# Kernel optimization log

Hardware: AMD Instinct MI355X
Metric: run time of the kernel (lower is better)

Reference implementation:

```python
import jax, jax.numpy as jnp
import numpy as np

N_LAYERS = 4
B, L, D = 2, 2048, 512
H, E = 8, 64          # n_heads = d_model // d_head
DFF = 1024
EPS = 1e-6
MAX_LOG_SCALE = float(np.log(100.0))   # QKNorm max_scale clamp
LOG10 = float(np.log(10.0))            # QKNorm scale init


def rms_norm(x, scale, eps=EPS):
    # matches torch rms_norm: x * (scale * rsqrt(mean(x^2, -1) + eps))
    ms = jnp.mean(jnp.square(x), axis=-1, keepdims=True)
    return x * (scale * jax.lax.rsqrt(ms + eps))


def rope(x):
    # standard rotary embedding over head dim, half-split convention. x: [n,h,l,e]
    e, l = x.shape[-1], x.shape[-2]
    inv = 1.0 / (10000.0 ** (jnp.arange(0, e, 2, dtype=jnp.float32) / e))
    freqs = jnp.arange(l, dtype=jnp.float32)[:, None] * inv[None, :]   # [l, e/2]
    cos, sin = jnp.cos(freqs), jnp.sin(freqs)
    x1, x2 = x[..., : e // 2], x[..., e // 2:]
    return jnp.concatenate([x1 * cos - x2 * sin, x1 * sin + x2 * cos], axis=-1)


def setup_inputs() -> dict:
    key = jax.random.key(0)
    ks = jax.random.split(key, 10)
    s = 0.02
    return {
        "x": jax.random.normal(ks[0], (B, L, D), jnp.float32),
        "cond": jax.random.normal(ks[1], (B, D), jnp.float32),
        "attn_mask": jnp.ones((B, L), jnp.int32),
        # per-layer stacked params (torch Linear(in,out,bias=False) stored as [in,out], y = x @ W)
        "wn_attn": s * jax.random.normal(ks[2], (N_LAYERS, D, D), jnp.float32),      # AdaRMSNorm cond proj (attn)
        "wqkv": s * jax.random.normal(ks[3], (N_LAYERS, D, 3 * D), jnp.float32),
        "qk_scale": jnp.full((N_LAYERS, H), LOG10, jnp.float32),                     # QKNorm per-head log-scale
        "wout": s * jax.random.normal(ks[4], (N_LAYERS, D, D), jnp.float32),
        "wn_ff": s * jax.random.normal(ks[5], (N_LAYERS, D, D), jnp.float32),        # AdaRMSNorm cond proj (ff)
        "wup": s * jax.random.normal(ks[6], (N_LAYERS, D, 2 * DFF), jnp.float32),
        "wdown": s * jax.random.normal(ks[7], (N_LAYERS, DFF, D), jnp.float32),
        "out_scale": jnp.ones((D,), jnp.float32),                                    # final RMSNorm scale
    }


def forward(x, cond, attn_mask, wn_attn, wqkv, qk_scale, wout, wn_ff, wup, wdown, out_scale):
    n, l, d = x.shape
    # mask bias: (attn_mask != 1) * -1e9, repeated 'n l -> n h l s' (query-dim mask, as in source)
    bias = (attn_mask != 1).astype(x.dtype) * -1e9
    bias = bias[:, None, :, None]  # [n,1,l,1] broadcast over heads and key dim

    def block(h_x, p):
        wn_a, w_qkv, qs, w_o, wn_f, w_up, w_dn = p
        # --- self attention ---
        skip = h_x
        y = rms_norm(h_x, (cond @ wn_a + 1.0)[:, None, :])            # AdaRMSNorm
        qkv = y @ w_qkv                                               # [n,l,3d]
        q, k, v = jnp.split(qkv, 3, axis=-1)
        to_heads = lambda t: t.reshape(n, l, H, E).transpose(0, 2, 1, 3)
        q, k, v = to_heads(q), to_heads(k), to_heads(v)
        qs_c = jnp.minimum(qs, MAX_LOG_SCALE)
        hs = jnp.exp(0.5 * qs_c - 0.25 * np.log(E))[:, None, None]    # [H,1,1] QKNorm scale
        q = rope(rms_norm(q, hs))
        k = rope(rms_norm(k, hs))
        scores = jnp.einsum('nhle,nhse->nhls', q, k) / np.sqrt(E) + bias
        attn = jax.nn.softmax(scores, axis=-1)
        o = jnp.einsum('nhls,nhse->nhle', attn, v)
        o = o.transpose(0, 2, 1, 3).reshape(n, l, d)
        h_x = skip + o @ w_o
        # --- GEGLU feed-forward ---
        skip = h_x
        y = rms_norm(h_x, (cond @ wn_f + 1.0)[:, None, :])
        u = y @ w_up
        a, b = jnp.split(u, 2, axis=-1)
        y = a * jax.nn.gelu(b, approximate=False)                     # F.gelu exact
        h_x = skip + y @ w_dn
        return h_x, None

    x, _ = jax.lax.scan(block, x, (wn_attn, wqkv, qk_scale, wout, wn_ff, wup, wdown))
    return rms_norm(x, out_scale)


def reference(x, cond, attn_mask, wn_attn, wqkv, qk_scale, wout, wn_ff, wup, wdown, out_scale):
    return forward(x, cond, attn_mask, wn_attn, wqkv, qk_scale, wout, wn_ff, wup, wdown, out_scale)
```

## Files before the change

kernel.cpp:

```cpp
#include <hip/hip_runtime.h>
#include <hip/hip_bf16.h>

#define NB 2
#define LL 2048
#define DD 512
#define HH 8
#define EE 64
#define DFF 1024
#define NL 4
#define EPS_F 1e-6f

typedef __bf16 bf16x8 __attribute__((ext_vector_type(8)));
typedef __bf16 bf16x4 __attribute__((ext_vector_type(4)));
typedef float f32x4 __attribute__((ext_vector_type(4)));

__device__ __forceinline__ unsigned short f2bf(float f) {
    unsigned int u = __float_as_uint(f);
    unsigned int r = (u + 0x7FFFu + ((u >> 16) & 1u)) >> 16;
    return (unsigned short)r;
}
__device__ __forceinline__ unsigned short f2bf_t(float f) {
    return (unsigned short)(__float_as_uint(f) >> 16);
}
__device__ __forceinline__ void gload16(const void* g, void* l) {
    __builtin_amdgcn_global_load_lds(
        (const __attribute__((address_space(1))) unsigned int*)g,
        (__attribute__((address_space(3))) unsigned int*)l, 16, 0, 0);
}

__global__ void rope_table_kernel(float* __restrict__ cosT, float* __restrict__ sinT) {
    int idx = blockIdx.x * 256 + threadIdx.x;
    if (idx >= LL * 32) return;
    int l = idx >> 5, i = idx & 31;
    float inv = powf(10000.f, -(float)i * (1.f / 32.f));
    float ang = (float)l * inv;
    cosT[idx] = cosf(ang);
    sinT[idx] = sinf(ang);
}

__global__ __launch_bounds__(256) void wcast_all_kernel(const float* __restrict__ wqkv,
                                                        const float* __restrict__ wout,
                                                        const float* __restrict__ wup,
                                                        const float* __restrict__ wdown,
                                                        unsigned short* __restrict__ wt) {
    int bid = blockIdx.x;
    int layer = bid / 2560, rem = bid % 2560;
    const float* W; unsigned short* WT; int K, N, t;
    if (rem < 768)       { W = wqkv  + (size_t)layer * 786432;  WT = wt + (size_t)layer * 786432;            K = 512;  N = 1536; t = rem; }
    else if (rem < 1024) { W = wout  + (size_t)layer * 262144;  WT = wt + 3145728 + (size_t)layer * 262144;  K = 512;  N = 512;  t = rem - 768; }
    else if (rem < 2048) { W = wup   + (size_t)layer * 1048576; WT = wt + 4194304 + (size_t)layer * 1048576; K = 512;  N = 2048; t = rem - 1024; }
    else                 { W = wdown + (size_t)layer * 524288;  WT = wt + 8388608 + (size_t)layer * 524288;  K = 1024; N = 512;  t = rem - 2048; }
    int tn = N / 32;
    int n0 = (t % tn) * 32, k0 = (t / tn) * 32;
    __shared__ float tile[32][33];
    int r = threadIdx.x >> 5, c = threadIdx.x & 31;
#pragma unroll
    for (int i = 0; i < 4; ++i)
        tile[r + 8 * i][c] = W[(size_t)(k0 + r + 8 * i) * N + n0 + c];
    __syncthreads();
#pragma unroll
    for (int i = 0; i < 4; ++i)
        WT[(size_t)(n0 + r + 8 * i) * K + k0 + c] = f2bf(tile[c][r + 8 * i]);
}

__global__ __launch_bounds__(256) void cond_all_kernel(const float* __restrict__ cond,
                                                       const float* __restrict__ wn_attn,
                                                       const float* __restrict__ wn_ff,
                                                       float* __restrict__ s_all) {
    int bid = blockIdx.x;
    int d0 = (bid & 7) * 64;
    int b = (bid >> 3) & 1;
    int which = (bid >> 4) & 1;
    int layer = bid >> 5;
    const float* W = (which ? wn_ff : wn_attn) + (size_t)layer * DD * DD;
    int t = threadIdx.x;
    int d = d0 + (t & 63), kq = t >> 6;
    const float* c = cond + b * DD + kq * 128;
    const float* Wp = W + (size_t)(kq * 128) * DD + d;
    float s = 0.f;
#pragma unroll 8
    for (int j = 0; j < 128; ++j) s = fmaf(c[j], Wp[(size_t)j * DD], s);
    __shared__ float red[4][64];
    red[kq][t & 63] = s;
    __syncthreads();
    if (t < 64) {
        float tot = 1.f + red[0][t] + red[1][t] + red[2][t] + red[3][t];
        s_all[((size_t)(layer * 2 + which) * NB + b) * DD + d0 + t] = tot;
    }
}

__global__ __launch_bounds__(256) void rmsnorm_bf16_kernel(const float* __restrict__ x,
                                                           const float* __restrict__ scale,
                                                           unsigned short* __restrict__ y) {
    int row = blockIdx.x;
    int b = row >> 11;
    int t = threadIdx.x;
    float2 v = ((const float2*)(x + (size_t)row * DD))[t];
    float ss = v.x * v.x + v.y * v.y;
#pragma unroll
    for (int o = 32; o > 0; o >>= 1) ss += __shfl_xor(ss, o);
    __shared__ float red[4];
    if ((t & 63) == 0) red[t >> 6] = ss;
    __syncthreads();
    float tot = red[0] + red[1] + red[2] + red[3];
    float inv = rsqrtf(tot * (1.f / DD) + EPS_F);
    float2 s2 = ((const float2*)(scale + b * DD))[t];
    unsigned int lo = f2bf(v.x * s2.x * inv);
    unsigned int hi = f2bf(v.y * s2.y * inv);
    ((unsigned int*)(y + (size_t)row * DD))[t] = lo | (hi << 16);
}

__global__ __launch_bounds__(256) void rmsnorm_f32_kernel(const float* __restrict__ x,
                                                          const float* __restrict__ scale,
                                                          float* __restrict__ y) {
    int row = blockIdx.x;
    int t = threadIdx.x;
    float2 v = ((const float2*)(x + (size_t)row * DD))[t];
    float ss = v.x * v.x + v.y * v.y;
#pragma unroll
    for (int o = 32; o > 0; o >>= 1) ss += __shfl_xor(ss, o);
    __shared__ float red[4];
    if ((t & 63) == 0) red[t >> 6] = ss;
    __syncthreads();
    float tot = red[0] + red[1] + red[2] + red[3];
    float inv = rsqrtf(tot * (1.f / DD) + EPS_F);
    float2 s2 = ((const float2*)scale)[t];
    float2 o2;
    o2.x = v.x * s2.x * inv;
    o2.y = v.y * s2.y * inv;
    ((float2*)(y + (size_t)row * DD))[t] = o2;
}

template <int BN>
__global__ __launch_bounds__(256) void gemm_bf16_kernel(const unsigned short* __restrict__ A,
                                                        const unsigned short* __restrict__ BT,
                                                        const float* __restrict__ R,
                                                        float* __restrict__ C,
                                                        int M, int N, int K) {
    constexpr int NJ = BN / 32;
    __shared__ __align__(16) unsigned short As[2][128 * 32];
    __shared__ __align__(16) unsigned short Bs[2][BN * 32];
    int tid = threadIdx.x;
    int n0 = blockIdx.x * BN, m0 = blockIdx.y * 128;
    int w = tid >> 6, l = tid & 63;
    int wr = w >> 1, wc = w & 1;
    int kf = 8 * (l >> 4);
    int rf = l & 15;

    auto stage = [&](int buf, int k0) {
#pragma unroll
        for (int u = 0; u < 2; ++u) {
            int c = u * 256 + tid;
            int row = c >> 2, ch = c & 3;
            gload16(A + (size_t)(m0 + row) * K + k0 + ch * 8, &As[buf][c * 8]);
        }
#pragma unroll
        for (int u = 0; u < BN / 64; ++u) {
            int c = u * 256 + tid;
            int row = c >> 2, ch = c & 3;
            gload16(BT + (size_t)(n0 + row) * K + k0 + ch * 8, &Bs[buf][c * 8]);
        }
    };

    f32x4 acc[4][NJ] = {};
    const int nt = K / 32;
    stage(0, 0);
    __syncthreads();

    for (int t = 0; t < nt; ++t) {
        if (t + 1 < nt) stage((t + 1) & 1, (t + 1) * 32);
        int cur = t & 1;
        bf16x8 a[4], b[NJ];
#pragma unroll
        for (int i = 0; i < 4; ++i)
            a[i] = *(const bf16x8*)(&As[cur][(wr * 64 + i * 16 + rf) * 32 + kf]);
#pragma unroll
        for (int j = 0; j < NJ; ++j)
            b[j] = *(const bf16x8*)(&Bs[cur][(wc * (BN / 2) + j * 16 + rf) * 32 + kf]);
#pragma unroll
        for (int i = 0; i < 4; ++i)
#pragma unroll
            for (int j = 0; j < NJ; ++j)
                acc[i][j] = __builtin_amdgcn_mfma_f32_16x16x32_bf16(a[i], b[j], acc[i][j], 0, 0, 0);
        __syncthreads();
    }

    int rl = l >> 4, cl = l & 15;
#pragma unroll
    for (int i = 0; i < 4; ++i)
#pragma unroll
        for (int j = 0; j < NJ; ++j)
#pragma unroll
            for (int r = 0; r < 4; ++r) {
                int row = m0 + wr * 64 + i * 16 + rl * 4 + r;
                int col = n0 + wc * (BN / 2) + j * 16 + cl;
                size_t off = (size_t)row * N + col;
                float v = acc[i][j][r];
                if (R) v += R[off];
                C[off] = v;
            }
}

__global__ __launch_bounds__(256) void gemm_geglu_kernel(const unsigned short* __restrict__ A,
                                                         const unsigned short* __restrict__ BT,
                                                         unsigned short* __restrict__ G) {
    __shared__ __align__(16) unsigned char smem[128 * 65 * sizeof(float)];
    unsigned short* As = (unsigned short*)smem;
    unsigned short* Bs = (unsigned short*)(smem + 16384);
    float* ep = (float*)smem;
    int tid = threadIdx.x;
    int n0 = blockIdx.x * 64, m0 = blockIdx.y * 128;
    int w = tid >> 6, l = tid & 63;
    int wr = w >> 1, wc = w & 1;
    int kf = 8 * (l >> 4);
    int rf = l & 15;

    auto stage = [&](int buf, int k0) {
#pragma unroll
        for (int u = 0; u < 2; ++u) {
            int c = u * 256 + tid;
            int row = c >> 2, ch = c & 3;
            gload16(A + (size_t)(m0 + row) * DD + k0 + ch * 8, &As[buf * 4096 + c * 8]);
            int grow = (row < 64) ? (n0 + row) : (DFF + n0 + row - 64);
            gload16(BT + (size_t)grow * DD + k0 + ch * 8, &Bs[buf * 4096 + c * 8]);
        }
    };

    f32x4 acc[4][4] = {};
    stage(0, 0);
    __syncthreads();

    for (int t = 0; t < 16; ++t) {
        if (t + 1 < 16) stage((t + 1) & 1, (t + 1) * 32);
        int cur = t & 1;
        bf16x8 a[4], b[4];
#pragma unroll
        for (int i = 0; i < 4; ++i)
            a[i] = *(const bf16x8*)(&As[cur * 4096 + (wr * 64 + i * 16 + rf) * 32 + kf]);
#pragma unroll
        for (int j = 0; j < 4; ++j)
            b[j] = *(const bf16x8*)(&Bs[cur * 4096 + (wc * 64 + j * 16 + rf) * 32 + kf]);
#pragma unroll
        for (int i = 0; i < 4; ++i)
#pragma unroll
            for (int j = 0; j < 4; ++j)
                acc[i][j] = __builtin_amdgcn_mfma_f32_16x16x32_bf16(a[i], b[j], acc[i][j], 0, 0, 0);
        __syncthreads();
    }

    int rl = l >> 4, cl = l & 15;
    if (wc == 0) {
#pragma unroll
        for (int i = 0; i < 4; ++i)
#pragma unroll
            for (int j = 0; j < 4; ++j)
#pragma unroll
                for (int r = 0; r < 4; ++r)
                    ep[(wr * 64 + i * 16 + rl * 4 + r) * 65 + j * 16 + cl] = acc[i][j][r];
    }
    __syncthreads();
    if (wc == 1) {
#pragma unroll
        for (int i = 0; i < 4; ++i)
#pragma unroll
            for (int j = 0; j < 4; ++j)
#pragma unroll
                for (int r = 0; r < 4; ++r) {
                    int row = wr * 64 + i * 16 + rl * 4 + r;
                    float bv = acc[i][j][r];
                    float av = ep[row * 65 + j * 16 + cl];
                    float ge = 0.5f * bv * (1.f + erff(bv * 0.70710678f));
                    G[(size_t)(m0 + row) * DFF + n0 + j * 16 + cl] = f2bf(av * ge);
                }
    }
}

__global__ __launch_bounds__(256) void qkv_prep_kernel(const float* __restrict__ qkv,
                                                       const float* __restrict__ qs,
                                                       const float* __restrict__ cosT,
                                                       const float* __restrict__ sinT,
                                                       unsigned short* __restrict__ qh,
                                                       unsigned short* __restrict__ kh,
                                                       unsigned short* __restrict__ vt) {
    __shared__ float tile[64][65];
    int t = threadIdx.x;
    if (blockIdx.x < 8192) {
        int w = blockIdx.x * 4 + (t >> 6);
        int e = t & 63;
        int h = w & 7;
        int l = (w >> 3) & (LL - 1);
        int b = w >> 14;
        size_t rb = ((size_t)(b * LL + l)) * (3 * DD) + h * EE + e;
        float q = qkv[rb];
        float k = qkv[rb + DD];
        float sq = q * q, sk = k * k;
#pragma unroll
        for (int o = 1; o < 64; o <<= 1) {
            sq += __shfl_xor(sq, o);
            sk += __shfl_xor(sk, o);
        }
        float hsc = expf(0.5f * fminf(qs[h], 4.60517019f) - 1.03972077f) * 0.35355339059f;
        float qn = q * (hsc * 1.44269504f) * rsqrtf(sq * (1.f / EE) + EPS_F);
        float kn = k * hsc * rsqrtf(sk * (1.f / EE) + EPS_F);
        float qp = __shfl_xor(qn, 32);
        float kp = __shfl_xor(kn, 32);
        int i = e & 31;
        float c = cosT[l * 32 + i], s = sinT[l * 32 + i];
        float qo = (e < 32) ? (qn * c - qp * s) : (qp * s + qn * c);
        float ko = (e < 32) ? (kn * c - kp * s) : (kp * s + kn * c);
        size_t ob = ((size_t)((b * HH + h) * LL + l)) * EE + e;
        qh[ob] = f2bf(qo);
        kh[ob] = f2bf(ko);
    } else {
        int bid = blockIdx.x - 8192;
        int lt = bid & 31, bh = bid >> 5;
        int b = bh >> 3, h = bh & 7;
        int l0 = lt * 64;
#pragma unroll
        for (int i = 0; i < 4; ++i) {
            int c = t + i * 256;
            int row = c >> 4, q4 = c & 15;
            float4 v4 = *(const float4*)(qkv + ((size_t)(b * LL + l0 + row)) * (3 * DD) + 2 * DD + h * EE + q4 * 4);
            tile[row][q4 * 4 + 0] = v4.x;
            tile[row][q4 * 4 + 1] = v4.y;
            tile[row][q4 * 4 + 2] = v4.z;
            tile[row][q4 * 4 + 3] = v4.w;
        }
        __syncthreads();
        int e = t >> 2, lc = t & 3;
        unsigned int* dst = (unsigned int*)(vt + ((size_t)(bh * EE + e)) * LL + l0 + lc * 16);
#pragma unroll
        for (int j2 = 0; j2 < 8; ++j2) {
            unsigned int lo = f2bf(tile[lc * 16 + 2 * j2][e]);
            unsigned int hi = f2bf(tile[lc * 16 + 2 * j2 + 1][e]);
            dst[j2] = lo | (hi << 16);
        }
    }
}

#define KVB 32
#define KLDP 72
#define VLDP 40
#define PLDP 36
__global__ __launch_bounds__(256) void flash_mfma_kernel(const unsigned short* __restrict__ qh,
                                                         const unsigned short* __restrict__ kh,
                                                         const unsigned short* __restrict__ vt,
                                                         float* __restrict__ op,
                                                         float* __restrict__ os) {
    __shared__ unsigned short K_lds[32 * KLDP];
    __shared__ unsigned short VT_lds[80 * VLDP];
    __shared__ unsigned short P_lds[4][16 * PLDP];
    int bid = blockIdx.x;
    int qb = bid & 31, h = (bid >> 5) & 7, b = (bid >> 8) & 1, split = bid >> 9;
    int bh = b * HH + h;
    int tid = threadIdx.x, w = tid >> 6, l = tid & 63;
    int lo = l & 15, hi4 = l >> 4;
    int q0 = qb * 64 + w * 16;

    for (int idx = tid; idx < 16 * VLDP; idx += 256) {
        int rr = idx / VLDP;
        VT_lds[(64 + rr) * VLDP + (idx - rr * VLDP)] = (rr == 0) ? 0x3F80 : 0;
    }

    const unsigned short* qbase = qh + ((size_t)bh * LL) * EE;
    bf16x8 qa[2];
#pragma unroll
    for (int s = 0; s < 2; ++s)
        qa[s] = *(const bf16x8*)(qbase + (size_t)(q0 + lo) * EE + s * 32 + 8 * hi4);

    f32x4 oacc[4] = {};
    f32x4 osum = {};

    for (int kt = split * 16; kt < split * 16 + 16; ++kt) {
        int kv0 = kt * KVB;
#pragma unroll
        for (int u = 0; u < 2; ++u) {
            int c = tid + u * 256;
            int arr = c >> 8, cc = c & 255;
            if (arr == 0) {
                int row = cc >> 3, ch = cc & 7;
                *(uint4*)&K_lds[row * KLDP + ch * 8] =
                    *(const uint4*)(kh + ((size_t)bh * LL + kv0 + row) * EE + ch * 8);
            } else {
                int row = cc >> 2, ch = cc & 3;
                *(uint4*)&VT_lds[row * VLDP + ch * 8] =
                    *(const uint4*)(vt + ((size_t)bh * EE + row) * LL + kv0 + ch * 8);
            }
        }
        __syncthreads();

        f32x4 S[2] = {};
        __builtin_amdgcn_s_setprio(1);
#pragma unroll
        for (int nf = 0; nf < 2; ++nf)
#pragma unroll
            for (int s = 0; s < 2; ++s) {
                bf16x8 kb = *(const bf16x8*)&K_lds[(nf * 16 + lo) * KLDP + s * 32 + 8 * hi4];
                S[nf] = __builtin_amdgcn_mfma_f32_16x16x32_bf16(qa[s], kb, S[nf], 0, 0, 0);
            }
        __builtin_amdgcn_s_setprio(0);

#pragma unroll
        for (int r = 0; r < 4; ++r)
#pragma unroll
            for (int nf = 0; nf < 2; ++nf)
                P_lds[w][(hi4 * 4 + r) * PLDP + nf * 16 + lo] = f2bf_t(exp2f(S[nf][r]));

        __builtin_amdgcn_s_setprio(1);
        bf16x4 p0 = *(const bf16x4*)&P_lds[w][lo * PLDP + 8 * hi4];
        bf16x4 p1 = *(const bf16x4*)&P_lds[w][lo * PLDP + 8 * hi4 + 4];
        bf16x8 pa;
#pragma unroll
        for (int j = 0; j < 4; ++j) { pa[j] = p0[j]; pa[4 + j] = p1[j]; }
#pragma unroll
        for (int nf = 0; nf < 4; ++nf) {
            bf16x8 vb = *(const bf16x8*)&VT_lds[(nf * 16 + lo) * VLDP + 8 * hi4];
            oacc[nf] = __builtin_amdgcn_mfma_f32_16x16x32_bf16(pa, vb, oacc[nf], 0, 0, 0);
        }
        bf16x8 vbE = *(const bf16x8*)&VT_lds[(64 + lo) * VLDP + 8 * hi4];
        osum = __builtin_amdgcn_mfma_f32_16x16x32_bf16(pa, vbE, osum, 0, 0, 0);
        __builtin_amdgcn_s_setprio(0);
        __syncthreads();
    }

    float* opp = op + (size_t)split * (NB * LL * DD);
#pragma unroll
    for (int r = 0; r < 4; ++r) {
        int row = q0 + hi4 * 4 + r;
        float* optr = opp + ((size_t)(b * LL + row)) * DD + h * EE;
#pragma unroll
        for (int nf = 0; nf < 4; ++nf)
            optr[nf * 16 + lo] = oacc[nf][r];
        if (lo == 0)
            os[split * (NB * HH * LL) + bh * LL + row] = osum[r];
    }
}

__global__ __launch_bounds__(256) void attn_combine_kernel(const float* __restrict__ op,
                                                           const float* __restrict__ os,
                                                           unsigned short* __restrict__ oh) {
    int idx = (blockIdx.x * 256 + threadIdx.x) * 4;
    int col = idx & 511;
    int h = col >> 6;
    int row = (idx >> 9) & (LL - 1);
    int b = idx >> 20;
    int bh = b * HH + h;
    float s = 0.f;
    float4 a = make_float4(0.f, 0.f, 0.f, 0.f);
#pragma unroll
    for (int sp = 0; sp < 4; ++sp) {
        s += os[sp * (NB * HH * LL) + bh * LL + row];
        float4 t = *(const float4*)(op + (size_t)sp * (NB * LL * DD) + idx);
        a.x += t.x; a.y += t.y; a.z += t.z; a.w += t.w;
    }
    float inv = 1.f / s;
    ushort4 o4;
    o4.x = f2bf(a.x * inv);
    o4.y = f2bf(a.y * inv);
    o4.z = f2bf(a.z * inv);
    o4.w = f2bf(a.w * inv);
    *(ushort4*)(oh + idx) = o4;
}

extern "C" void kernel_launch(void* const* d_in, const int* in_sizes, int n_in,
                              void* d_out, int out_size, void* d_ws, size_t ws_size,
                              hipStream_t stream) {
    const float* x        = (const float*)d_in[0];
    const float* cond     = (const float*)d_in[1];
    const float* wn_attn  = (const float*)d_in[3];
    const float* wqkv     = (const float*)d_in[4];
    const float* qk_scale = (const float*)d_in[5];
    const float* wout     = (const float*)d_in[6];
    const float* wn_ff    = (const float*)d_in[7];
    const float* wup      = (const float*)d_in[8];
    const float* wdown    = (const float*)d_in[9];
    const float* out_scale= (const float*)d_in[10];
    float* out = (float*)d_out;

    const int TOK = NB * LL;
    const size_t nHx = (size_t)TOK * DD;
    const size_t M = 1024 * 1024;

    float* ws = (float*)d_ws;
    float* hx  = ws;
    unsigned short* y_bf = (unsigned short*)(ws + 2 * M);
    float* qkv = ws + 3 * M;
    float* op  = ws + 3 * M;
    unsigned short* qh_bf = (unsigned short*)(ws + 11 * M);
    unsigned short* g_bf  = (unsigned short*)(ws + 11 * M);
    unsigned short* kh_bf = (unsigned short*)(ws + 12 * M);
    unsigned short* vt_bf = (unsigned short*)(ws + 13 * M);
    unsigned short* oh_bf = (unsigned short*)(ws + 14 * M);
    unsigned short* wt = (unsigned short*)(ws + 15 * M);
    float* smal  = ws + 20 * M;
    float* s_all = smal;
    float* os    = smal + 8192;
    float* cosT  = os + 131072;
    float* sinT  = cosT + 65536;

    hipMemcpyAsync(hx, x, nHx * sizeof(float), hipMemcpyDeviceToDevice, stream);
    rope_table_kernel<<<256, 256, 0, stream>>>(cosT, sinT);
    cond_all_kernel<<<128, 256, 0, stream>>>(cond, wn_attn, wn_ff, s_all);
    wcast_all_kernel<<<10240, 256, 0, stream>>>(wqkv, wout, wup, wdown, wt);

    unsigned short* wqkvT  = wt;
    unsigned short* woutT  = wt + 3145728;
    unsigned short* wupT   = wt + 4194304;
    unsigned short* wdownT = wt + 8388608;

    for (int layer = 0; layer < NL; ++layer) {
        const float* qs = qk_scale + layer * HH;

        rmsnorm_bf16_kernel<<<TOK, 256, 0, stream>>>(hx, s_all + (size_t)(layer * 2 + 0) * NB * DD, y_bf);
        gemm_bf16_kernel<64><<<dim3(1536 / 64, TOK / 128), 256, 0, stream>>>(
            y_bf, wqkvT + (size_t)layer * 786432, nullptr, qkv, TOK, 1536, 512);
        qkv_prep_kernel<<<8704, 256, 0, stream>>>(qkv, qs, cosT, sinT, qh_bf, kh_bf, vt_bf);
        flash_mfma_kernel<<<2048, 256, 0, stream>>>(qh_bf, kh_bf, vt_bf, op, os);
        attn_combine_kernel<<<2048, 256, 0, stream>>>(op, os, oh_bf);
        gemm_bf16_kernel<64><<<dim3(512 / 64, TOK / 128), 256, 0, stream>>>(
            oh_bf, woutT + (size_t)layer * 262144, hx, hx, TOK, 512, 512);

        rmsnorm_bf16_kernel<<<TOK, 256, 0, stream>>>(hx, s_all + (size_t)(layer * 2 + 1) * NB * DD, y_bf);
        gemm_geglu_kernel<<<dim3(16, 32), 256, 0, stream>>>(
            y_bf, wupT + (size_t)layer * 1048576, g_bf);
        gemm_bf16_kernel<64><<<dim3(512 / 64, TOK / 128), 256, 0, stream>>>(
            g_bf, wdownT + (size_t)layer * 524288, hx, hx, TOK, 512, 1024);
    }
    rmsnorm_f32_kernel<<<TOK, 256, 0, stream>>>(hx, out_scale, out);
}
```

Before: 614.3 us.

## Fuse QKV GEMM with QK-norm/RoPE/V-transpose epilogue and store split-K partials in bf16

The QKV projection GEMM now applies per-head RMS norm, the QKNorm scale and RoPE in its epilogue, and writes q/k head layouts and the transposed V directly. This removes the fp32 qkv intermediate and the separate prep kernel. The flash-attention split partial outputs are also stored as bf16 instead of fp32, which halves the partial-output traffic read by the combine kernel, now vectorized 8-wide. The cost is lower precision in the unnormalized partial sums and extra LDS and shuffle work inside the GEMM epilogue.

Result: faster. 577.7 us (-6.0%).

```diff
diff --git a/kernel.cpp b/kernel.cpp
--- a/kernel.cpp
+++ b/kernel.cpp
@@ -201,6 +201,107 @@
             }
 }
 
+__global__ __launch_bounds__(256) void gemm_qkv_fused_kernel(const unsigned short* __restrict__ A,
+                                                             const unsigned short* __restrict__ BT,
+                                                             const float* __restrict__ qs,
+                                                             const float* __restrict__ cosT,
+                                                             const float* __restrict__ sinT,
+                                                             unsigned short* __restrict__ qh,
+                                                             unsigned short* __restrict__ kh,
+                                                             unsigned short* __restrict__ vt) {
+    __shared__ __align__(16) unsigned char smem[128 * 65 * sizeof(float)];
+    unsigned short* As = (unsigned short*)smem;
+    unsigned short* Bs = (unsigned short*)(smem + 16384);
+    float* ex = (float*)smem;
+    int tid = threadIdx.x;
+    int ct = blockIdx.x, m0 = blockIdx.y * 128;
+    int n0 = ct * 64;
+    int w = tid >> 6, l = tid & 63;
+    int wr = w >> 1, wc = w & 1;
+    int kf = 8 * (l >> 4);
+    int rf = l & 15;
+
+    auto stage = [&](int buf, int k0) {
+#pragma unroll
+        for (int u = 0; u < 2; ++u) {
+            int c = u * 256 + tid;
+            int row = c >> 2, ch = c & 3;
+            gload16(A + (size_t)(m0 + row) * DD + k0 + ch * 8, &As[buf * 4096 + c * 8]);
+        }
+        int c = tid;
+        int row = c >> 2, ch = c & 3;
+        gload16(BT + (size_t)(n0 + row) * DD + k0 + ch * 8, &Bs[buf * 2048 + c * 8]);
+    };
+
+    f32x4 acc[4][2] = {};
+    stage(0, 0);
+    __syncthreads();
+    for (int t = 0; t < 16; ++t) {
+        if (t + 1 < 16) stage((t + 1) & 1, (t + 1) * 32);
+        int cur = t & 1;
+        bf16x8 a[4], b[2];
+#pragma unroll
+        for (int i = 0; i < 4; ++i)
+            a[i] = *(const bf16x8*)(&As[cur * 4096 + (wr * 64 + i * 16 + rf) * 32 + kf]);
+#pragma unroll
+        for (int j = 0; j < 2; ++j)
+            b[j] = *(const bf16x8*)(&Bs[cur * 2048 + (wc * 32 + j * 16 + rf) * 32 + kf]);
+#pragma unroll
+        for (int i = 0; i < 4; ++i)
+#pragma unroll
+            for (int j = 0; j < 2; ++j)
+                acc[i][j] = __builtin_amdgcn_mfma_f32_16x16x32_bf16(a[i], b[j], acc[i][j], 0, 0, 0);
+        __syncthreads();
+    }
+
+    int rl = l >> 4, cl = l & 15;
+#pragma unroll
+    for (int i = 0; i < 4; ++i)
+#pragma unroll
+        for (int j = 0; j < 2; ++j)
+#pragma unroll
+            for (int r = 0; r < 4; ++r)
+                ex[(wr * 64 + i * 16 + rl * 4 + r) * 65 + wc * 32 + j * 16 + cl] = acc[i][j][r];
+    __syncthreads();
+
+    int b = m0 >> 11;
+    int lbase = m0 & (LL - 1);
+    if (ct < 16) {
+        int h = ct & 7;
+        bool isq = ct < 8;
+        float hsc = expf(0.5f * fminf(qs[h], 4.60517019f) - 1.03972077f) * 0.35355339059f;
+        if (isq) hsc *= 1.44269504f;
+        unsigned short* dst = (isq ? qh : kh) + ((size_t)(b * HH + h) * LL) * EE;
+#pragma unroll 4
+        for (int it = 0; it < 32; ++it) {
+            int row = w * 32 + it;
+            int lloc = lbase + row;
+            float v = ex[row * 65 + l];
+            float ss = v * v;
+#pragma unroll
+            for (int d = 1; d < 64; d <<= 1) ss += __shfl_xor(ss, d);
+            float inv = hsc * rsqrtf(ss * (1.f / EE) + EPS_F);
+            float pr = ex[row * 65 + (l ^ 32)];
+            int i2 = l & 31;
+            float c = cosT[lloc * 32 + i2], s = sinT[lloc * 32 + i2];
+            float vn = v * inv, pn = pr * inv;
+            float o = (l < 32) ? (vn * c - pn * s) : (pn * s + vn * c);
+            dst[(size_t)lloc * EE + l] = f2bf(o);
+        }
+    } else {
+        int h = ct - 16;
+        int bh = b * HH + h;
+#pragma unroll 4
+        for (int it = 0; it < 16; ++it) {
+            int e = w * 16 + it;
+            float v0 = ex[(2 * l) * 65 + e];
+            float v1 = ex[(2 * l + 1) * 65 + e];
+            unsigned int pk = (unsigned int)f2bf(v0) | ((unsigned int)f2bf(v1) << 16);
+            *(unsigned int*)(vt + ((size_t)(bh * EE + e)) * LL + lbase + 2 * l) = pk;
+        }
+    }
+}
+
 __global__ __launch_bounds__(256) void gemm_geglu_kernel(const unsigned short* __restrict__ A,
                                                          const unsigned short* __restrict__ BT,
                                                          unsigned short* __restrict__ G) {
@@ -275,69 +376,6 @@
     }
 }
 
-__global__ __launch_bounds__(256) void qkv_prep_kernel(const float* __restrict__ qkv,
-                                                       const float* __restrict__ qs,
-                                                       const float* __restrict__ cosT,
-                                                       const float* __restrict__ sinT,
-                                                       unsigned short* __restrict__ qh,
-                                                       unsigned short* __restrict__ kh,
-                                                       unsigned short* __restrict__ vt) {
-    __shared__ float tile[64][65];
-    int t = threadIdx.x;
-    if (blockIdx.x < 8192) {
-        int w = blockIdx.x * 4 + (t >> 6);
-        int e = t & 63;
-        int h = w & 7;
-        int l = (w >> 3) & (LL - 1);
-        int b = w >> 14;
-        size_t rb = ((size_t)(b * LL + l)) * (3 * DD) + h * EE + e;
-        float q = qkv[rb];
-        float k = qkv[rb + DD];
-        float sq = q * q, sk = k * k;
-#pragma unroll
-        for (int o = 1; o < 64; o <<= 1) {
-            sq += __shfl_xor(sq, o);
-            sk += __shfl_xor(sk, o);
-        }
-        float hsc = expf(0.5f * fminf(qs[h], 4.60517019f) - 1.03972077f) * 0.35355339059f;
-        float qn = q * (hsc * 1.44269504f) * rsqrtf(sq * (1.f / EE) + EPS_F);
-        float kn = k * hsc * rsqrtf(sk * (1.f / EE) + EPS_F);
-        float qp = __shfl_xor(qn, 32);
-        float kp = __shfl_xor(kn, 32);
-        int i = e & 31;
-        float c = cosT[l * 32 + i], s = sinT[l * 32 + i];
-        float qo = (e < 32) ? (qn * c - qp * s) : (qp * s + qn * c);
-        float ko = (e < 32) ? (kn * c - kp * s) : (kp * s + kn * c);
-        size_t ob = ((size_t)((b * HH + h) * LL + l)) * EE + e;
-        qh[ob] = f2bf(qo);
-        kh[ob] = f2bf(ko);
-    } else {
-        int bid = blockIdx.x - 8192;
-        int lt = bid & 31, bh = bid >> 5;
-        int b = bh >> 3, h = bh & 7;
-        int l0 = lt * 64;
-#pragma unroll
-        for (int i = 0; i < 4; ++i) {
-            int c = t + i * 256;
-            int row = c >> 4, q4 = c & 15;
-            float4 v4 = *(const float4*)(qkv + ((size_t)(b * LL + l0 + row)) * (3 * DD) + 2 * DD + h * EE + q4 * 4);
-            tile[row][q4 * 4 + 0] = v4.x;
-            tile[row][q4 * 4 + 1] = v4.y;
-            tile[row][q4 * 4 + 2] = v4.z;
-            tile[row][q4 * 4 + 3] = v4.w;
-        }
-        __syncthreads();
-        int e = t >> 2, lc = t & 3;
-        unsigned int* dst = (unsigned int*)(vt + ((size_t)(bh * EE + e)) * LL + l0 + lc * 16);
-#pragma unroll
-        for (int j2 = 0; j2 < 8; ++j2) {
-            unsigned int lo = f2bf(tile[lc * 16 + 2 * j2][e]);
-            unsigned int hi = f2bf(tile[lc * 16 + 2 * j2 + 1][e]);
-            dst[j2] = lo | (hi << 16);
-        }
-    }
-}
-
 #define KVB 32
 #define KLDP 72
 #define VLDP 40
@@ -345,7 +383,7 @@
 __global__ __launch_bounds__(256) void flash_mfma_kernel(const unsigned short* __restrict__ qh,
                                                          const unsigned short* __restrict__ kh,
                                                          const unsigned short* __restrict__ vt,
-                                                         float* __restrict__ op,
+                                                         unsigned short* __restrict__ op,
                                                          float* __restrict__ os) {
     __shared__ unsigned short K_lds[32 * KLDP];
     __shared__ unsigned short VT_lds[80 * VLDP];
@@ -423,43 +461,48 @@
         __syncthreads();
     }
 
-    float* opp = op + (size_t)split * (NB * LL * DD);
+    unsigned short* opp = op + (size_t)split * (NB * LL * DD);
 #pragma unroll
     for (int r = 0; r < 4; ++r) {
         int row = q0 + hi4 * 4 + r;
-        float* optr = opp + ((size_t)(b * LL + row)) * DD + h * EE;
+        unsigned short* optr = opp + ((size_t)(b * LL + row)) * DD + h * EE;
 #pragma unroll
         for (int nf = 0; nf < 4; ++nf)
-            optr[nf * 16 + lo] = oacc[nf][r];
+            optr[nf * 16 + lo] = f2bf(oacc[nf][r]);
         if (lo == 0)
             os[split * (NB * HH * LL) + bh * LL + row] = osum[r];
     }
 }
 
-__global__ __launch_bounds__(256) void attn_combine_kernel(const float* __restrict__ op,
+__global__ __launch_bounds__(256) void attn_combine_kernel(const unsigned short* __restrict__ op,
                                                            const float* __restrict__ os,
                                                            unsigned short* __restrict__ oh) {
-    int idx = (blockIdx.x * 256 + threadIdx.x) * 4;
+    int idx = (blockIdx.x * 256 + threadIdx.x) * 8;
     int col = idx & 511;
     int h = col >> 6;
     int row = (idx >> 9) & (LL - 1);
     int b = idx >> 20;
     int bh = b * HH + h;
     float s = 0.f;
-    float4 a = make_float4(0.f, 0.f, 0.f, 0.f);
+    float a[8] = {};
 #pragma unroll
     for (int sp = 0; sp < 4; ++sp) {
         s += os[sp * (NB * HH * LL) + bh * LL + row];
-        float4 t = *(const float4*)(op + (size_t)sp * (NB * LL * DD) + idx);
-        a.x += t.x; a.y += t.y; a.z += t.z; a.w += t.w;
+        uint4 t = *(const uint4*)(op + (size_t)sp * (NB * LL * DD) + idx);
+        unsigned int dw[4] = {t.x, t.y, t.z, t.w};
+#pragma unroll
+        for (int j = 0; j < 4; ++j) {
+            a[2 * j]     += __uint_as_float(dw[j] << 16);
+            a[2 * j + 1] += __uint_as_float(dw[j] & 0xFFFF0000u);
+        }
     }
     float inv = 1.f / s;
-    ushort4 o4;
-    o4.x = f2bf(a.x * inv);
-    o4.y = f2bf(a.y * inv);
-    o4.z = f2bf(a.z * inv);
-    o4.w = f2bf(a.w * inv);
-    *(ushort4*)(oh + idx) = o4;
+    uint4 o4;
+    unsigned int* po = (unsigned int*)&o4;
+#pragma unroll
+    for (int j = 0; j < 4; ++j)
+        po[j] = (unsigned int)f2bf(a[2 * j] * inv) | ((unsigned int)f2bf(a[2 * j + 1] * inv) << 16);
+    *(uint4*)(oh + idx) = o4;
 }
 
 extern "C" void kernel_launch(void* const* d_in, const int* in_sizes, int n_in,
@@ -484,8 +527,7 @@
     float* ws = (float*)d_ws;
     float* hx  = ws;
     unsigned short* y_bf = (unsigned short*)(ws + 2 * M);
-    float* qkv = ws + 3 * M;
-    float* op  = ws + 3 * M;
+    unsigned short* op   = (unsigned short*)(ws + 3 * M);
     unsigned short* qh_bf = (unsigned short*)(ws + 11 * M);
     unsigned short* g_bf  = (unsigned short*)(ws + 11 * M);
     unsigned short* kh_bf = (unsigned short*)(ws + 12 * M);
@@ -512,11 +554,10 @@
         const float* qs = qk_scale + layer * HH;
 
         rmsnorm_bf16_kernel<<<TOK, 256, 0, stream>>>(hx, s_all + (size_t)(layer * 2 + 0) * NB * DD, y_bf);
-        gemm_bf16_kernel<64><<<dim3(1536 / 64, TOK / 128), 256, 0, stream>>>(
-            y_bf, wqkvT + (size_t)layer * 786432, nullptr, qkv, TOK, 1536, 512);
-        qkv_prep_kernel<<<8704, 256, 0, stream>>>(qkv, qs, cosT, sinT, qh_bf, kh_bf, vt_bf);
+        gemm_qkv_fused_kernel<<<dim3(24, TOK / 128), 256, 0, stream>>>(
+            y_bf, wqkvT + (size_t)layer * 786432, qs, cosT, sinT, qh_bf, kh_bf, vt_bf);
         flash_mfma_kernel<<<2048, 256, 0, stream>>>(qh_bf, kh_bf, vt_bf, op, os);
-        attn_combine_kernel<<<2048, 256, 0, stream>>>(op, os, oh_bf);
+        attn_combine_kernel<<<1024, 256, 0, stream>>>(op, os, oh_bf);
         gemm_bf16_kernel<64><<<dim3(512 / 64, TOK / 128), 256, 0, stream>>>(
             oh_bf, woutT + (size_t)layer * 262144, hx, hx, TOK, 512, 512);
 
```
